# Kernel tuning notes

Hardware: AMD Instinct MI355X
Metric: run time of the kernel (lower is better)

The kernel has to match this reference:

```python
import jax, jax.numpy as jnp
import numpy as np
import math

B, C, IMG, P = 32, 4, 32, 2
D, H, L = 768, 12, 12
HD = D // H
HID = 4 * D
NCLS = 10
NP_ = (IMG // P) ** 2  # 256 patches


def setup_inputs() -> dict:
    key = jax.random.key(0)
    ks = iter(jax.random.split(key, 40))
    s = 0.02
    rn = lambda shape: jax.random.normal(next(ks), shape, dtype=jnp.float32) * s
    inp = {
        "x": jax.random.normal(next(ks), (B, C, IMG, IMG), dtype=jnp.float32),
        "t": jax.random.uniform(next(ks), (B,), dtype=jnp.float32),
        "conv_w": rn((D, C, P, P)), "conv_b": rn((D,)),
        "tmlp_w1": rn((D, 4 * D)), "tmlp_b1": rn((4 * D,)),
        "tmlp_w2": rn((4 * D, D)), "tmlp_b2": rn((D,)),
        "cls_emb": rn((NCLS + 1, D)),
        "qkv_w": rn((L, D, 3 * D)), "qkv_b": rn((L, 3 * D)),
        "outp_w": rn((L, D, D)), "outp_b": rn((L, D)),
        "ada_w": rn((L, D, 6 * D)), "ada_b": rn((L, 6 * D)),
        "mlp_w1": rn((L, D, HID)), "mlp_b1": rn((L, HID)),
        "mlp_w2": rn((L, HID, D)), "mlp_b2": rn((L, D)),
        "fin_ada_w": rn((D, 2 * D)), "fin_ada_b": rn((2 * D,)),
        "fin_lin_w": rn((D, P * P * C)), "fin_lin_b": rn((P * P * C,)),
        "class_label": jax.random.randint(next(ks), (B,), 0, NCLS + 1),
    }
    return inp


def _layer_norm(x, eps=1e-6):
    m = jnp.mean(x, axis=-1, keepdims=True)
    v = jnp.mean((x - m) ** 2, axis=-1, keepdims=True)
    return (x - m) * jax.lax.rsqrt(v + eps)


def _pos_embed():
    pos = jnp.arange(NP_, dtype=jnp.float32)[:, None]
    dim = jnp.arange(0, D, 2, dtype=jnp.float32)
    ang = pos / jnp.power(10000.0, dim / D)
    pe = jnp.zeros((NP_, D), dtype=jnp.float32)
    pe = pe.at[:, 0::2].set(jnp.sin(ang)).at[:, 1::2].set(jnp.cos(ang))
    return pe[None]


def _time_embed(t):
    half = D // 2
    emb = jnp.exp(jnp.arange(half, dtype=jnp.float32) * -(math.log(10000.0) / (half - 1)))
    e = t[:, None] * emb[None, :]
    return jnp.concatenate([jnp.sin(e), jnp.cos(e)], axis=-1)


def _forward(x, t, class_label, conv_w, conv_b, tmlp_w1, tmlp_b1, tmlp_w2, tmlp_b2,
             cls_emb, qkv_w, qkv_b, outp_w, outp_b, ada_w, ada_b,
             mlp_w1, mlp_b1, mlp_w2, mlp_b2, fin_ada_w, fin_ada_b, fin_lin_w, fin_lin_b):
    h = IMG // P
    # patchify (stride==kernel conv == reshape + matmul)
    xp = x.reshape(B, C, h, P, h, P).transpose(0, 2, 4, 1, 3, 5).reshape(B, NP_, C * P * P)
    tok = xp @ conv_w.reshape(D, C * P * P).T + conv_b  # [B,N,D]
    tok = tok + _pos_embed()

    c = _time_embed(t)
    c = jax.nn.silu(c @ tmlp_w1 + tmlp_b1) @ tmlp_w2 + tmlp_b2
    c = c + cls_emb[class_label]  # [B,D]

    scale = 1.0 / math.sqrt(HD)
    for i in range(L):
        ada = jax.nn.silu(c) @ ada_w[i] + ada_b[i]  # [B,6D]
        sh1, sc1, g1, sh2, sc2, g2 = jnp.split(ada, 6, axis=-1)
        # attention branch
        hmod = _layer_norm(tok) * (1 + sc1[:, None]) + sh1[:, None]
        qkv = (hmod @ qkv_w[i] + qkv_b[i]).reshape(B, NP_, 3, H, HD)
        q, k, v = [qkv[:, :, j].transpose(0, 2, 1, 3) for j in range(3)]  # [B,H,N,hd]
        attn = jax.nn.softmax(jnp.einsum('bhnd,bhmd->bhnm', q, k) * scale, axis=-1)
        o = jnp.einsum('bhnm,bhmd->bhnd', attn, v).transpose(0, 2, 1, 3).reshape(B, NP_, D)
        tok = tok + g1[:, None] * (o @ outp_w[i] + outp_b[i])
        # mlp branch
        hmod = _layer_norm(tok) * (1 + sc2[:, None]) + sh2[:, None]
        hmid = jax.nn.gelu(hmod @ mlp_w1[i] + mlp_b1[i], approximate=False)
        tok = tok + g2[:, None] * (hmid @ mlp_w2[i] + mlp_b2[i])

    ada = jax.nn.silu(c) @ fin_ada_w + fin_ada_b
    shf, scf = jnp.split(ada, 2, axis=-1)
    tok = _layer_norm(tok) * (1 + scf[:, None]) + shf[:, None]
    out = tok @ fin_lin_w + fin_lin_b  # [B,N,p*p*C]
    # unpatchify
    out = out.reshape(B, h, h, P, P, C).transpose(0, 5, 1, 3, 2, 4).reshape(B, C, h * P, h * P)
    return out


def reference(x, t, conv_w, conv_b, tmlp_w1, tmlp_b1, tmlp_w2, tmlp_b2, cls_emb,
              qkv_w, qkv_b, outp_w, outp_b, ada_w, ada_b, mlp_w1, mlp_b1, mlp_w2, mlp_b2,
              fin_ada_w, fin_ada_b, fin_lin_w, fin_lin_b, class_label):
    return _forward(x, t, class_label, conv_w, conv_b, tmlp_w1, tmlp_b1, tmlp_w2, tmlp_b2,
                    cls_emb, qkv_w, qkv_b, outp_w, outp_b, ada_w, ada_b,
                    mlp_w1, mlp_b1, mlp_w2, mlp_b2, fin_ada_w, fin_ada_b, fin_lin_w, fin_lin_b)
```

## Files before the change

### kernel.cpp

```cpp
#include <hip/hip_runtime.h>
#include <math.h>

#define NB    32
#define D     768
#define NPP   256
#define NTOK  (NB*NPP)
#define NHEAD 12
#define NLAY  12
#define ADA6  4608

typedef unsigned short bf16_t;
typedef __attribute__((ext_vector_type(8))) short  bf16x8;
typedef __attribute__((ext_vector_type(4))) float  f32x4;

__device__ __forceinline__ float silu_f(float x){ return x / (1.f + __expf(-x)); }
__device__ __forceinline__ float gelu_f(float x){ return 0.5f*x*(1.f + erff(x*0.7071067811865476f)); }

__device__ __forceinline__ bf16_t f2bf(float f){
  unsigned int u; __builtin_memcpy(&u, &f, 4);
  unsigned int r = (u + 0x7fffu + ((u >> 16) & 1u)) >> 16;
  return (bf16_t)r;
}
__device__ __forceinline__ float bf2f(unsigned int bits){
  unsigned int u = bits << 16; float f; __builtin_memcpy(&f, &u, 4); return f;
}

__device__ __forceinline__ void stf(float* p, float v){ *p = v; }
__device__ __forceinline__ void stf(bf16_t* p, float v){ *p = f2bf(v); }

#define GLD16(gsrc, ldst) __builtin_amdgcn_global_load_lds( \
    (const __attribute__((address_space(1))) void*)(gsrc), \
    (__attribute__((address_space(3))) void*)(ldst), 16, 0, 0)

__global__ void k_patchify(const float* __restrict__ x, const float* __restrict__ cw,
                           const float* __restrict__ cb, float* __restrict__ tok){
  int idx = blockIdx.x*256 + threadIdx.x;
  int d = idx % D, tk = idx / D;
  int b = tk >> 8, n = tk & 255;
  int hi = n >> 4, wi = n & 15;
  float acc = cb[d];
  const float* xb = x + (size_t)b*4*32*32;
  #pragma unroll
  for (int c=0;c<4;c++)
    #pragma unroll
    for (int p1=0;p1<2;p1++)
      #pragma unroll
      for (int p2=0;p2<2;p2++){
        float xv = xb[(c*32 + hi*2+p1)*32 + wi*2+p2];
        acc = fmaf(xv, cw[d*16 + c*4 + p1*2 + p2], acc);
      }
  int i2 = d >> 1;
  float ang = (float)n * powf(10000.f, -(float)(2*i2)/768.f);
  acc += (d & 1) ? cosf(ang) : sinf(ang);
  tok[idx] = acc;
}

__global__ void k_timeembed(const float* __restrict__ t, float* __restrict__ c0){
  int idx = blockIdx.x*256 + threadIdx.x;
  if (idx >= NB*D) return;
  int b = idx / D, d = idx % D;
  int j = (d < 384) ? d : d - 384;
  float emb = expf((float)j * (-logf(10000.f)/383.f));
  float e = t[b]*emb;
  c0[idx] = (d < 384) ? sinf(e) : cosf(e);
}

__global__ void k_silu(const float* __restrict__ in, float* __restrict__ out, int n){
  int i = blockIdx.x*256 + threadIdx.x;
  if (i < n) out[i] = silu_f(in[i]);
}

template<int EPI>
__global__ void k_gemm_small(const float* __restrict__ A, const float* __restrict__ W,
                             const float* __restrict__ bias, float* __restrict__ Cout,
                             int N, int K,
                             const float* __restrict__ cls, const int* __restrict__ label){
  int n = blockIdx.x*256 + threadIdx.x;
  int m = blockIdx.y;
  if (n >= N) return;
  const float* a = A + (size_t)m*K;
  float acc = bias[n];
  #pragma unroll 4
  for (int k=0;k<K;k++) acc = fmaf(a[k], W[(size_t)k*N + n], acc);
  if (EPI==1) acc = silu_f(acc);
  if (EPI==2) acc += cls[(size_t)label[m]*D + n];
  Cout[(size_t)m*N + n] = acc;
}

template<typename OT>
__global__ void k_lnmod(const float* __restrict__ tok, const float* __restrict__ ada,
                        OT* __restrict__ outb, int ada_stride, int sh_off, int sc_off){
  int tk = blockIdx.x, tid = threadIdx.x;
  int b = tk >> 8;
  const float* row = tok + (size_t)tk*D;
  float x0 = row[tid], x1 = row[tid+256], x2 = row[tid+512];
  float s1 = x0+x1+x2;
  float s2 = x0*x0 + x1*x1 + x2*x2;
  #pragma unroll
  for (int off=32; off; off>>=1){
    s1 += __shfl_xor(s1, off);
    s2 += __shfl_xor(s2, off);
  }
  __shared__ float r1[4], r2[4];
  int wid = tid >> 6, lane = tid & 63;
  if (lane==0){ r1[wid]=s1; r2[wid]=s2; }
  __syncthreads();
  float t1 = r1[0]+r1[1]+r1[2]+r1[3];
  float t2 = r2[0]+r2[1]+r2[2]+r2[3];
  float mean = t1*(1.f/768.f);
  float var  = t2*(1.f/768.f) - mean*mean;
  float rstd = rsqrtf(var + 1e-6f);
  const float* sh = ada + (size_t)b*ada_stride + sh_off;
  const float* sc = ada + (size_t)b*ada_stride + sc_off;
  OT* orow = outb + (size_t)tk*D;
  stf(&orow[tid    ], (x0-mean)*rstd*(1.f+sc[tid    ]) + sh[tid    ]);
  stf(&orow[tid+256], (x1-mean)*rstd*(1.f+sc[tid+256]) + sh[tid+256]);
  stf(&orow[tid+512], (x2-mean)*rstd*(1.f+sc[tid+512]) + sh[tid+512]);
}

__global__ void k_w2bf16t(const float* __restrict__ W, bf16_t* __restrict__ Wt,
                          int K, int N){
  __shared__ float t[32][33];
  int n0 = blockIdx.x*32, k0 = blockIdx.y*32;
  int c = threadIdx.x & 31, r0 = threadIdx.x >> 5;
  #pragma unroll
  for (int rr=0; rr<4; rr++){
    int r = r0 + rr*8;
    t[r][c] = W[(size_t)(k0+r)*N + n0 + c];
  }
  __syncthreads();
  #pragma unroll
  for (int rr=0; rr<4; rr++){
    int r = r0 + rr*8;
    Wt[(size_t)(n0+r)*K + k0 + c] = f2bf(t[c][r]);
  }
}

template<int EPI>
__launch_bounds__(256)
__global__ void k_gemm_mfma(const bf16_t* __restrict__ A, const bf16_t* __restrict__ Wt,
                            const float* __restrict__ bias, bf16_t* __restrict__ Cout,
                            float* __restrict__ tokio, int N, int K,
                            const float* __restrict__ adap, int gate_off){
  __shared__ bf16_t As[128*32];
  __shared__ bf16_t Bs[128*32];
  int tid = threadIdx.x;
  int w = tid >> 6, lane = tid & 63;
  int col0 = blockIdx.x*128, row0 = blockIdx.y*128;
  int wm = w >> 1, wn = w & 1;

  int sRow = lane >> 2;
  int sK   = (lane & 3) * 8;

  f32x4 acc[4][4];
  #pragma unroll
  for (int i=0;i<4;i++)
    #pragma unroll
    for (int j=0;j<4;j++)
      acc[i][j] = (f32x4){0.f,0.f,0.f,0.f};

  const bf16_t* Aptr = A  + (size_t)row0*K;
  const bf16_t* Bptr = Wt + (size_t)col0*K;
  int fr = lane & 15, g = lane >> 4;

  for (int kt=0; kt<K; kt+=32){
    #pragma unroll
    for (int r=0;r<2;r++){
      int ch = w*2 + r;
      int rowi = ch*16 + sRow;
      GLD16(Aptr + (size_t)rowi*K + kt + sK, As + ch*512);
      GLD16(Bptr + (size_t)rowi*K + kt + sK, Bs + ch*512);
    }
    __syncthreads();
    bf16x8 af[4], bfr[4];
    #pragma unroll
    for (int i=0;i<4;i++)
      af[i] = *(const bf16x8*)&As[(wm*64 + i*16 + fr)*32 + g*8];
    #pragma unroll
    for (int j=0;j<4;j++)
      bfr[j] = *(const bf16x8*)&Bs[(wn*64 + j*16 + fr)*32 + g*8];
    #pragma unroll
    for (int i=0;i<4;i++)
      #pragma unroll
      for (int j=0;j<4;j++)
        acc[i][j] = __builtin_amdgcn_mfma_f32_16x16x32_bf16(af[i], bfr[j], acc[i][j], 0, 0, 0);
    __syncthreads();
  }

  int g4 = g*4;
  int bb = row0 >> 8;
  #pragma unroll
  for (int i=0;i<4;i++){
    #pragma unroll
    for (int j=0;j<4;j++){
      int c = col0 + wn*64 + j*16 + fr;
      float bv = bias[c];
      float gv = 0.f;
      if (EPI==2) gv = adap[(size_t)bb*ADA6 + gate_off + c];
      #pragma unroll
      for (int v=0; v<4; v++){
        int r = row0 + wm*64 + i*16 + g4 + v;
        float val = acc[i][j][v] + bv;
        if (EPI==0) Cout[(size_t)r*N + c] = f2bf(val);
        if (EPI==1) Cout[(size_t)r*N + c] = f2bf(gelu_f(val));
        if (EPI==2) tokio[(size_t)r*N + c] += gv*val;
      }
    }
  }
}

__launch_bounds__(256)
__global__ void k_attn(const bf16_t* __restrict__ qkv, bf16_t* __restrict__ o){
  int bh = blockIdx.x;
  int b = bh / NHEAD, h = bh % NHEAD;
  int tid = threadIdx.x;
  __shared__ float Ks[256][64];
  __shared__ float Vs[256][64];
  const bf16_t* base = qkv + (size_t)b*NPP*2304;
  #pragma unroll
  for (int p=0;p<8;p++){
    int gidx = p*256 + tid;
    int r = gidx >> 3, c8 = gidx & 7;
    uint4 kv = *(const uint4*)(base + (size_t)r*2304 + 768  + h*64 + c8*8);
    uint4 vv = *(const uint4*)(base + (size_t)r*2304 + 1536 + h*64 + c8*8);
    float* kd = &Ks[r][c8*8];
    float* vd = &Vs[r][c8*8];
    kd[0]=bf2f(kv.x&0xffff); kd[1]=bf2f(kv.x>>16); kd[2]=bf2f(kv.y&0xffff); kd[3]=bf2f(kv.y>>16);
    kd[4]=bf2f(kv.z&0xffff); kd[5]=bf2f(kv.z>>16); kd[6]=bf2f(kv.w&0xffff); kd[7]=bf2f(kv.w>>16);
    vd[0]=bf2f(vv.x&0xffff); vd[1]=bf2f(vv.x>>16); vd[2]=bf2f(vv.y&0xffff); vd[3]=bf2f(vv.y>>16);
    vd[4]=bf2f(vv.z&0xffff); vd[5]=bf2f(vv.z>>16); vd[6]=bf2f(vv.w&0xffff); vd[7]=bf2f(vv.w>>16);
  }
  float q[64];
  const bf16_t* qrow = base + (size_t)tid*2304 + h*64;
  #pragma unroll
  for (int d8=0; d8<8; d8++){
    uint4 qv = *(const uint4*)(qrow + d8*8);
    float* qd = &q[d8*8];
    qd[0]=bf2f(qv.x&0xffff)*0.125f; qd[1]=bf2f(qv.x>>16)*0.125f;
    qd[2]=bf2f(qv.y&0xffff)*0.125f; qd[3]=bf2f(qv.y>>16)*0.125f;
    qd[4]=bf2f(qv.z&0xffff)*0.125f; qd[5]=bf2f(qv.z>>16)*0.125f;
    qd[6]=bf2f(qv.w&0xffff)*0.125f; qd[7]=bf2f(qv.w>>16)*0.125f;
  }
  __syncthreads();

  float m = -1e30f, l = 0.f;
  float acc[64];
  #pragma unroll
  for (int d=0; d<64; d++) acc[d]=0.f;

  for (int k=0;k<256;k++){
    const float4* krow = (const float4*)&Ks[k][0];
    float s0=0.f,s1=0.f,s2=0.f,s3=0.f;
    #pragma unroll
    for (int d4=0; d4<16; d4++){
      float4 kv = krow[d4];
      s0 = fmaf(q[d4*4+0], kv.x, s0);
      s1 = fmaf(q[d4*4+1], kv.y, s1);
      s2 = fmaf(q[d4*4+2], kv.z, s2);
      s3 = fmaf(q[d4*4+3], kv.w, s3);
    }
    float s = (s0+s1)+(s2+s3);
    float mn = fmaxf(m, s);
    float corr = __expf(m - mn);
    float p = __expf(s - mn);
    l = l*corr + p;
    m = mn;
    const float4* vrow = (const float4*)&Vs[k][0];
    #pragma unroll
    for (int d4=0; d4<16; d4++){
      float4 vv = vrow[d4];
      acc[d4*4+0] = fmaf(acc[d4*4+0], corr, p*vv.x);
      acc[d4*4+1] = fmaf(acc[d4*4+1], corr, p*vv.y);
      acc[d4*4+2] = fmaf(acc[d4*4+2], corr, p*vv.z);
      acc[d4*4+3] = fmaf(acc[d4*4+3], corr, p*vv.w);
    }
  }
  float inv = 1.f/l;
  bf16_t* orow = o + (size_t)(b*NPP + tid)*D + h*64;
  #pragma unroll
  for (int d8=0; d8<8; d8++){
    uint4 sv;
    sv.x = (unsigned)f2bf(acc[d8*8+0]*inv) | ((unsigned)f2bf(acc[d8*8+1]*inv)<<16);
    sv.y = (unsigned)f2bf(acc[d8*8+2]*inv) | ((unsigned)f2bf(acc[d8*8+3]*inv)<<16);
    sv.z = (unsigned)f2bf(acc[d8*8+4]*inv) | ((unsigned)f2bf(acc[d8*8+5]*inv)<<16);
    sv.w = (unsigned)f2bf(acc[d8*8+6]*inv) | ((unsigned)f2bf(acc[d8*8+7]*inv)<<16);
    *(uint4*)(orow + d8*8) = sv;
  }
}

__global__ void k_final(const float* __restrict__ tokf, const float* __restrict__ w,
                        const float* __restrict__ bias, float* __restrict__ out){
  int idx = blockIdx.x*256 + threadIdx.x;
  int j = idx & 15, tk = idx >> 4;
  const float* a = tokf + (size_t)tk*D;
  float acc = bias[j];
  #pragma unroll 4
  for (int k=0;k<D;k++) acc = fmaf(a[k], w[k*16 + j], acc);
  int b = tk >> 8, n = tk & 255;
  int hi = n >> 4, wi = n & 15;
  int p1 = j >> 3, p2 = (j >> 2) & 1, c = j & 3;
  out[((size_t)(b*4 + c)*32 + hi*2 + p1)*32 + wi*2 + p2] = acc;
}

extern "C" void kernel_launch(void* const* d_in, const int* in_sizes, int n_in,
                              void* d_out, int out_size, void* d_ws, size_t ws_size,
                              hipStream_t stream){
  const float* x         = (const float*)d_in[0];
  const float* t         = (const float*)d_in[1];
  const float* conv_w    = (const float*)d_in[2];
  const float* conv_b    = (const float*)d_in[3];
  const float* tmlp_w1   = (const float*)d_in[4];
  const float* tmlp_b1   = (const float*)d_in[5];
  const float* tmlp_w2   = (const float*)d_in[6];
  const float* tmlp_b2   = (const float*)d_in[7];
  const float* cls_emb   = (const float*)d_in[8];
  const float* qkv_w     = (const float*)d_in[9];
  const float* qkv_b     = (const float*)d_in[10];
  const float* outp_w    = (const float*)d_in[11];
  const float* outp_b    = (const float*)d_in[12];
  const float* ada_w     = (const float*)d_in[13];
  const float* ada_b     = (const float*)d_in[14];
  const float* mlp_w1    = (const float*)d_in[15];
  const float* mlp_b1    = (const float*)d_in[16];
  const float* mlp_w2    = (const float*)d_in[17];
  const float* mlp_b2    = (const float*)d_in[18];
  const float* fin_ada_w = (const float*)d_in[19];
  const float* fin_ada_b = (const float*)d_in[20];
  const float* fin_lin_w = (const float*)d_in[21];
  const float* fin_lin_b = (const float*)d_in[22];
  const int*   label     = (const int*)d_in[23];
  float* out = (float*)d_out;

  char* wp = (char*)d_ws;
  float*  tok   = (float*)wp;              wp += (size_t)NTOK*D*4;
  bf16_t* bigb  = (bf16_t*)wp;             wp += (size_t)NTOK*3072*2;
  bf16_t* hmodb = (bf16_t*)wp;             wp += (size_t)NTOK*D*2;
  bf16_t* oattb = (bf16_t*)wp;             wp += (size_t)NTOK*D*2;
  bf16_t* wqT   = (bf16_t*)wp;             wp += (size_t)2304*768*2;
  bf16_t* woT   = (bf16_t*)wp;             wp += (size_t)768*768*2;
  bf16_t* w1T   = (bf16_t*)wp;             wp += (size_t)3072*768*2;
  bf16_t* w2T   = (bf16_t*)wp;             wp += (size_t)768*3072*2;
  float*  c0    = (float*)wp;              wp += (size_t)NB*D*4;
  float*  chid  = (float*)wp;              wp += (size_t)NB*3072*4;
  float*  cvec  = (float*)wp;              wp += (size_t)NB*D*4;
  float*  scv   = (float*)wp;              wp += (size_t)NB*D*4;
  float*  ada   = (float*)wp;              wp += (size_t)NB*ADA6*4;
  float*  fada  = (float*)wp;              wp += (size_t)NB*1536*4;
  float*  hmodF = (float*)bigb;

  k_patchify<<<NTOK*D/256, 256, 0, stream>>>(x, conv_w, conv_b, tok);
  k_timeembed<<<(NB*D)/256, 256, 0, stream>>>(t, c0);
  k_gemm_small<1><<<dim3(3072/256, NB), 256, 0, stream>>>(c0, tmlp_w1, tmlp_b1, chid, 3072, 768, nullptr, nullptr);
  k_gemm_small<2><<<dim3(768/256, NB), 256, 0, stream>>>(chid, tmlp_w2, tmlp_b2, cvec, 768, 3072, cls_emb, label);
  k_silu<<<(NB*D)/256, 256, 0, stream>>>(cvec, scv, NB*D);

  for (int i=0;i<NLAY;i++){
    const float* qw  = qkv_w  + (size_t)i*768*2304;
    const float* qb  = qkv_b  + (size_t)i*2304;
    const float* ow  = outp_w + (size_t)i*768*768;
    const float* ob  = outp_b + (size_t)i*768;
    const float* aw  = ada_w  + (size_t)i*768*ADA6;
    const float* ab  = ada_b  + (size_t)i*ADA6;
    const float* m1w = mlp_w1 + (size_t)i*768*3072;
    const float* m1b = mlp_b1 + (size_t)i*3072;
    const float* m2w = mlp_w2 + (size_t)i*3072*768;
    const float* m2b = mlp_b2 + (size_t)i*768;

    k_w2bf16t<<<dim3(2304/32,  768/32), 256, 0, stream>>>(qw,  wqT, 768, 2304);
    k_w2bf16t<<<dim3( 768/32,  768/32), 256, 0, stream>>>(ow,  woT, 768, 768);
    k_w2bf16t<<<dim3(3072/32,  768/32), 256, 0, stream>>>(m1w, w1T, 768, 3072);
    k_w2bf16t<<<dim3( 768/32, 3072/32), 256, 0, stream>>>(m2w, w2T, 3072, 768);

    k_gemm_small<0><<<dim3(ADA6/256, NB), 256, 0, stream>>>(scv, aw, ab, ada, ADA6, 768, nullptr, nullptr);
    k_lnmod<bf16_t><<<NTOK, 256, 0, stream>>>(tok, ada, hmodb, ADA6, 0, 768);
    k_gemm_mfma<0><<<dim3(2304/128, NTOK/128), 256, 0, stream>>>(hmodb, wqT, qb, bigb, nullptr, 2304, 768, nullptr, 0);
    k_attn<<<NB*NHEAD, 256, 0, stream>>>(bigb, oattb);
    k_gemm_mfma<2><<<dim3( 768/128, NTOK/128), 256, 0, stream>>>(oattb, woT, ob, nullptr, tok, 768, 768, ada, 1536);
    k_lnmod<bf16_t><<<NTOK, 256, 0, stream>>>(tok, ada, hmodb, ADA6, 2304, 3072);
    k_gemm_mfma<1><<<dim3(3072/128, NTOK/128), 256, 0, stream>>>(hmodb, w1T, m1b, bigb, nullptr, 3072, 768, nullptr, 0);
    k_gemm_mfma<2><<<dim3( 768/128, NTOK/128), 256, 0, stream>>>(bigb, w2T, m2b, nullptr, tok, 768, 3072, ada, 3840);
  }

  k_gemm_small<0><<<dim3(1536/256, NB), 256, 0, stream>>>(scv, fin_ada_w, fin_ada_b, fada, 1536, 768, nullptr, nullptr);
  k_lnmod<float><<<NTOK, 256, 0, stream>>>(tok, fada, hmodF, 1536, 0, 768);
  k_final<<<NTOK*16/256, 256, 0, stream>>>(hmodF, fin_lin_w, fin_lin_b, out);
}
```

Before: 8.990 ms.

## Batch all adaLN projections into one skinny GEMM with split-K reduction

Replaces the per-layer small GEMM for the adaLN modulation vectors with a single launch that computes every layer's modulation up front. The final adaLN projection is also hoisted into that prologue. The new skinny GEMM caches the input row in shared memory and splits K across four wavefronts, then reduces the partial sums through shared memory. This raises parallelism for the tiny-M GEMMs and removes twelve serialized low-occupancy launches. In exchange it needs a larger workspace buffer, and the consumers now index into it with a layer offset and leading dimension.

```diff
diff --git a/kernel.cpp b/kernel.cpp
--- a/kernel.cpp
+++ b/kernel.cpp
@@ -8,6 +8,7 @@
 #define NHEAD 12
 #define NLAY  12
 #define ADA6  4608
+#define ADATOT (NLAY*ADA6)
 
 typedef unsigned short bf16_t;
 typedef __attribute__((ext_vector_type(8))) short  bf16x8;
@@ -71,20 +72,40 @@
 }
 
 template<int EPI>
-__global__ void k_gemm_small(const float* __restrict__ A, const float* __restrict__ W,
-                             const float* __restrict__ bias, float* __restrict__ Cout,
-                             int N, int K,
-                             const float* __restrict__ cls, const int* __restrict__ label){
-  int n = blockIdx.x*256 + threadIdx.x;
+__launch_bounds__(256)
+__global__ void k_gemm_skinny(const float* __restrict__ A, const float* __restrict__ W,
+                              const float* __restrict__ bias, float* __restrict__ Cout,
+                              int Ntot, int Nper, int K,
+                              const float* __restrict__ cls, const int* __restrict__ label){
+  __shared__ float Als[3072];
+  __shared__ float red[4][64];
+  int tid = threadIdx.x;
   int m = blockIdx.y;
-  if (n >= N) return;
-  const float* a = A + (size_t)m*K;
-  float acc = bias[n];
+  int j = tid & 63;
+  int ng = blockIdx.x*64 + j;
+  int ks = tid >> 6;
+  int lay = ng / Nper;
+  int n   = ng - lay*Nper;
+  const float* arow = A + (size_t)m*K;
+  for (int k = tid; k < K; k += 256) Als[k] = arow[k];
+  __syncthreads();
+  const float* wcol = W + (size_t)lay*K*Nper + n;
+  int kq = K >> 2;
+  int k0 = ks*kq;
+  float acc = 0.f;
   #pragma unroll 4
-  for (int k=0;k<K;k++) acc = fmaf(a[k], W[(size_t)k*N + n], acc);
-  if (EPI==1) acc = silu_f(acc);
-  if (EPI==2) acc += cls[(size_t)label[m]*D + n];
-  Cout[(size_t)m*N + n] = acc;
+  for (int kk = 0; kk < kq; kk++){
+    int k = k0 + kk;
+    acc = fmaf(Als[k], wcol[(size_t)k*Nper], acc);
+  }
+  red[ks][j] = acc;
+  __syncthreads();
+  if (ks == 0){
+    float s = red[0][j] + red[1][j] + red[2][j] + red[3][j] + bias[ng];
+    if (EPI==1) s = silu_f(s);
+    if (EPI==2) s += cls[(size_t)label[m]*D + n];
+    Cout[(size_t)m*Ntot + ng] = s;
+  }
 }
 
 template<typename OT>
@@ -141,7 +162,7 @@
 __global__ void k_gemm_mfma(const bf16_t* __restrict__ A, const bf16_t* __restrict__ Wt,
                             const float* __restrict__ bias, bf16_t* __restrict__ Cout,
                             float* __restrict__ tokio, int N, int K,
-                            const float* __restrict__ adap, int gate_off){
+                            const float* __restrict__ adap, int ada_ld, int gate_off){
   __shared__ bf16_t As[128*32];
   __shared__ bf16_t Bs[128*32];
   int tid = threadIdx.x;
@@ -196,7 +217,7 @@
       int c = col0 + wn*64 + j*16 + fr;
       float bv = bias[c];
       float gv = 0.f;
-      if (EPI==2) gv = adap[(size_t)bb*ADA6 + gate_off + c];
+      if (EPI==2) gv = adap[(size_t)bb*ada_ld + gate_off + c];
       #pragma unroll
       for (int v=0; v<4; v++){
         int r = row0 + wm*64 + i*16 + g4 + v;
@@ -332,56 +353,55 @@
   float* out = (float*)d_out;
 
   char* wp = (char*)d_ws;
-  float*  tok   = (float*)wp;              wp += (size_t)NTOK*D*4;
-  bf16_t* bigb  = (bf16_t*)wp;             wp += (size_t)NTOK*3072*2;
-  bf16_t* hmodb = (bf16_t*)wp;             wp += (size_t)NTOK*D*2;
-  bf16_t* oattb = (bf16_t*)wp;             wp += (size_t)NTOK*D*2;
-  bf16_t* wqT   = (bf16_t*)wp;             wp += (size_t)2304*768*2;
-  bf16_t* woT   = (bf16_t*)wp;             wp += (size_t)768*768*2;
-  bf16_t* w1T   = (bf16_t*)wp;             wp += (size_t)3072*768*2;
-  bf16_t* w2T   = (bf16_t*)wp;             wp += (size_t)768*3072*2;
-  float*  c0    = (float*)wp;              wp += (size_t)NB*D*4;
-  float*  chid  = (float*)wp;              wp += (size_t)NB*3072*4;
-  float*  cvec  = (float*)wp;              wp += (size_t)NB*D*4;
-  float*  scv   = (float*)wp;              wp += (size_t)NB*D*4;
-  float*  ada   = (float*)wp;              wp += (size_t)NB*ADA6*4;
-  float*  fada  = (float*)wp;              wp += (size_t)NB*1536*4;
-  float*  hmodF = (float*)bigb;
+  float*  tok     = (float*)wp;    wp += (size_t)NTOK*D*4;
+  bf16_t* bigb    = (bf16_t*)wp;   wp += (size_t)NTOK*3072*2;
+  bf16_t* hmodb   = (bf16_t*)wp;   wp += (size_t)NTOK*D*2;
+  bf16_t* oattb   = (bf16_t*)wp;   wp += (size_t)NTOK*D*2;
+  bf16_t* wqT     = (bf16_t*)wp;   wp += (size_t)2304*768*2;
+  bf16_t* woT     = (bf16_t*)wp;   wp += (size_t)768*768*2;
+  bf16_t* w1T     = (bf16_t*)wp;   wp += (size_t)3072*768*2;
+  bf16_t* w2T     = (bf16_t*)wp;   wp += (size_t)768*3072*2;
+  float*  c0      = (float*)wp;    wp += (size_t)NB*D*4;
+  float*  chid    = (float*)wp;    wp += (size_t)NB*3072*4;
+  float*  cvec    = (float*)wp;    wp += (size_t)NB*D*4;
+  float*  scv     = (float*)wp;    wp += (size_t)NB*D*4;
+  float*  ada_all = (float*)wp;    wp += (size_t)NB*ADATOT*4;
+  float*  fada    = (float*)wp;    wp += (size_t)NB*1536*4;
+  float*  hmodF   = (float*)bigb;
 
   k_patchify<<<NTOK*D/256, 256, 0, stream>>>(x, conv_w, conv_b, tok);
   k_timeembed<<<(NB*D)/256, 256, 0, stream>>>(t, c0);
-  k_gemm_small<1><<<dim3(3072/256, NB), 256, 0, stream>>>(c0, tmlp_w1, tmlp_b1, chid, 3072, 768, nullptr, nullptr);
-  k_gemm_small<2><<<dim3(768/256, NB), 256, 0, stream>>>(chid, tmlp_w2, tmlp_b2, cvec, 768, 3072, cls_emb, label);
+  k_gemm_skinny<1><<<dim3(3072/64, NB), 256, 0, stream>>>(c0,   tmlp_w1, tmlp_b1, chid, 3072, 3072, 768,  nullptr, nullptr);
+  k_gemm_skinny<2><<<dim3( 768/64, NB), 256, 0, stream>>>(chid, tmlp_w2, tmlp_b2, cvec,  768,  768, 3072, cls_emb, label);
   k_silu<<<(NB*D)/256, 256, 0, stream>>>(cvec, scv, NB*D);
+  k_gemm_skinny<0><<<dim3(ADATOT/64, NB), 256, 0, stream>>>(scv, ada_w, ada_b, ada_all, ADATOT, ADA6, 768, nullptr, nullptr);
+  k_gemm_skinny<0><<<dim3(1536/64, NB), 256, 0, stream>>>(scv, fin_ada_w, fin_ada_b, fada, 1536, 1536, 768, nullptr, nullptr);
 
   for (int i=0;i<NLAY;i++){
     const float* qw  = qkv_w  + (size_t)i*768*2304;
     const float* qb  = qkv_b  + (size_t)i*2304;
     const float* ow  = outp_w + (size_t)i*768*768;
     const float* ob  = outp_b + (size_t)i*768;
-    const float* aw  = ada_w  + (size_t)i*768*ADA6;
-    const float* ab  = ada_b  + (size_t)i*ADA6;
     const float* m1w = mlp_w1 + (size_t)i*768*3072;
     const float* m1b = mlp_b1 + (size_t)i*3072;
     const float* m2w = mlp_w2 + (size_t)i*3072*768;
     const float* m2b = mlp_b2 + (size_t)i*768;
+    int ao = i*ADA6;
 
     k_w2bf16t<<<dim3(2304/32,  768/32), 256, 0, stream>>>(qw,  wqT, 768, 2304);
     k_w2bf16t<<<dim3( 768/32,  768/32), 256, 0, stream>>>(ow,  woT, 768, 768);
     k_w2bf16t<<<dim3(3072/32,  768/32), 256, 0, stream>>>(m1w, w1T, 768, 3072);
     k_w2bf16t<<<dim3( 768/32, 3072/32), 256, 0, stream>>>(m2w, w2T, 3072, 768);
 
-    k_gemm_small<0><<<dim3(ADA6/256, NB), 256, 0, stream>>>(scv, aw, ab, ada, ADA6, 768, nullptr, nullptr);
-    k_lnmod<bf16_t><<<NTOK, 256, 0, stream>>>(tok, ada, hmodb, ADA6, 0, 768);
-    k_gemm_mfma<0><<<dim3(2304/128, NTOK/128), 256, 0, stream>>>(hmodb, wqT, qb, bigb, nullptr, 2304, 768, nullptr, 0);
+    k_lnmod<bf16_t><<<NTOK, 256, 0, stream>>>(tok, ada_all, hmodb, ADATOT, ao+0, ao+768);
+    k_gemm_mfma<0><<<dim3(2304/128, NTOK/128), 256, 0, stream>>>(hmodb, wqT, qb, bigb, nullptr, 2304, 768, nullptr, 0, 0);
     k_attn<<<NB*NHEAD, 256, 0, stream>>>(bigb, oattb);
-    k_gemm_mfma<2><<<dim3( 768/128, NTOK/128), 256, 0, stream>>>(oattb, woT, ob, nullptr, tok, 768, 768, ada, 1536);
-    k_lnmod<bf16_t><<<NTOK, 256, 0, stream>>>(tok, ada, hmodb, ADA6, 2304, 3072);
-    k_gemm_mfma<1><<<dim3(3072/128, NTOK/128), 256, 0, stream>>>(hmodb, w1T, m1b, bigb, nullptr, 3072, 768, nullptr, 0);
-    k_gemm_mfma<2><<<dim3( 768/128, NTOK/128), 256, 0, stream>>>(bigb, w2T, m2b, nullptr, tok, 768, 3072, ada, 3840);
-  }
-
-  k_gemm_small<0><<<dim3(1536/256, NB), 256, 0, stream>>>(scv, fin_ada_w, fin_ada_b, fada, 1536, 768, nullptr, nullptr);
+    k_gemm_mfma<2><<<dim3( 768/128, NTOK/128), 256, 0, stream>>>(oattb, woT, ob, nullptr, tok, 768, 768, ada_all, ADATOT, ao+1536);
+    k_lnmod<bf16_t><<<NTOK, 256, 0, stream>>>(tok, ada_all, hmodb, ADATOT, ao+2304, ao+3072);
+    k_gemm_mfma<1><<<dim3(3072/128, NTOK/128), 256, 0, stream>>>(hmodb, w1T, m1b, bigb, nullptr, 3072, 768, nullptr, 0, 0);
+    k_gemm_mfma<2><<<dim3( 768/128, NTOK/128), 256, 0, stream>>>(bigb, w2T, m2b, nullptr, tok, 768, 3072, ada_all, ADATOT, ao+3840);
+  }
+
   k_lnmod<float><<<NTOK, 256, 0, stream>>>(tok, fada, hmodF, 1536, 0, 768);
   k_final<<<NTOK*16/256, 256, 0, stream>>>(hmodF, fin_lin_w, fin_lin_b, out);
 }
```

New measurement: 8.377 ms. -6.8%, faster.
